# Kernel optimization log

Measured on AMD Instinct MI355X. Metric: run time of the kernel, lower is better.

Reference implementation:

```python
import jax, jax.numpy as jnp
import numpy as np

# dims
B, N, D = 4, 1024, 768
H, HD = 12, 64            # num_heads, head_dim (routed q heads = top-H experts)
EA = 24                   # num_attn_experts
EF, KF = 8, 2             # num_ffd_experts, ffd_heads (top-k for FFN MoE)
HS = int(4 * D) // KF     # ffn expert head_size = 1536
T = 9                     # task_num
S = 1                     # shared FFN experts: max(1, int(8*0.1))


def layernorm(x, g, b, eps=1e-5):
    m = x.mean(-1, keepdims=True)
    v = ((x - m) ** 2).mean(-1, keepdims=True)
    return (x - m) * jax.lax.rsqrt(v + eps) * g + b


def setup_inputs() -> dict:
    key = jax.random.key(0)
    ks = jax.random.split(key, 16)
    s = 0.02
    rn = lambda k, shp: jax.random.normal(k, shp, dtype=jnp.float32)
    return {
        "x": rn(ks[0], (B, N, D)),
        "task_bh": 3,
        "ln1_g": jnp.ones((D,), jnp.float32), "ln1_b": jnp.zeros((D,), jnp.float32),
        "ln2_g": jnp.ones((D,), jnp.float32), "ln2_b": jnp.zeros((D,), jnp.float32),
        "gate_a": rn(ks[1], (T, D, EA)) * s,
        "Wq_in": rn(ks[2], (EA, D, HD)) * s,
        "Wq_out": rn(ks[3], (EA, HD, D)) * s,
        "W_kv": rn(ks[4], (D, 2 * HD)) * s, "b_kv": jnp.zeros((2 * HD,), jnp.float32),
        "gate_f": rn(ks[5], (T, D, EF)) * s,
        "W1f": rn(ks[6], (EF, D, HS)) * s, "b1f": jnp.zeros((EF, HS), jnp.float32),
        "W2f": rn(ks[7], (EF, HS, D)) * s, "b_out": jnp.zeros((D,), jnp.float32),
        "Ws1": rn(ks[8], (S, D, HS)) * s, "bs1": jnp.zeros((S, HS), jnp.float32),
        "Ws2": rn(ks[9], (S, HS, D)) * s,
    }


def _route(h, gate_w, k):
    # h: [B,N,D], gate_w: [D,E] -> normalized top-k weights + one-hot dispatch
    probs = jax.nn.softmax(jnp.einsum("bnd,de->bne", h, gate_w), axis=-1)
    topv, topi = jax.lax.top_k(probs, k)                 # [B,N,k]
    topv = topv / topv.sum(-1, keepdims=True)
    oh = jax.nn.one_hot(topi, probs.shape[-1], dtype=h.dtype)  # [B,N,k,E]
    return topv, oh


def reference(x, task_bh, ln1_g, ln1_b, ln2_g, ln2_b, gate_a, Wq_in, Wq_out,
              W_kv, b_kv, gate_f, W1f, b1f, W2f, b_out, Ws1, bs1, Ws2):
    # --- MoE attention (routed q heads, shared single-head k/v) ---
    h = layernorm(x, ln1_g, ln1_b)
    topv, oh = _route(h, gate_a[task_bh], H)             # [B,N,H], [B,N,H,EA]
    h_all = jnp.einsum("bnd,edh->bneh", h, Wq_in)        # all-expert q projections
    q = jnp.einsum("bnke,bneh->bnkh", oh, h_all)         # gathered q heads [B,N,H,HD]
    kv = h @ W_kv + b_kv
    kk, vv = kv[..., :HD], kv[..., HD:]                  # [B,N,HD]
    att = jnp.einsum("bihd,bjd->bhij", q, kk) * (HD ** -0.5)
    att = jax.nn.softmax(att, axis=-1)
    o = jnp.einsum("bhij,bjd->bihd", att, vv)            # [B,N,H,HD]
    dense = jnp.einsum("bnk,bnke,bnkh->bneh", topv, oh, o)  # scatter to experts
    y = jnp.einsum("bneh,ehd->bnd", dense, Wq_out)       # gated expert output proj
    x = x + y

    # --- MoE FFN (top-KF routed experts + shared experts) ---
    h = layernorm(x, ln2_g, ln2_b)
    topv, oh = _route(h, gate_f[task_bh], KF)            # [B,N,KF], [B,N,KF,EF]
    h_all = jax.nn.gelu(jnp.einsum("bnd,edh->bneh", h, W1f) + b1f, approximate=False)
    wdense = jnp.einsum("bnk,bnke->bne", topv, oh)       # per-expert gate weights
    y = jnp.einsum("bne,bneh,ehd->bnd", wdense, h_all, W2f) + b_out
    hs = jax.nn.gelu(jnp.einsum("bnd,sdh->bnsh", h, Ws1) + bs1, approximate=False)
    y = y + jnp.einsum("bnsh,shd->bnd", hs, Ws2)         # always-on shared experts
    return x + y
```

## Files before the change

kernel.cpp:

```cpp
#include <hip/hip_runtime.h>
#include <hip/hip_bf16.h>

#define NTOK 4096
#define DDIM 768
#define NEA  24
#define NHEAD 12
#define HDIM 64
#define NEF  8
#define HSD  1536
#define SEQL 1024
#define NB   4
#define MAXTILE 104
#define NQKV 1664

using bf16 = __hip_bfloat16;

typedef float v4f __attribute__((ext_vector_type(4)));
typedef short v8s __attribute__((ext_vector_type(8)));
typedef __bf16 v8bf __attribute__((ext_vector_type(8)));

typedef __attribute__((address_space(3))) unsigned lds_u32_t;
typedef const __attribute__((address_space(1))) unsigned glb_u32_t;

__device__ __forceinline__ void gload16(const void* g, void* l) {
  __builtin_amdgcn_global_load_lds((glb_u32_t*)g, (lds_u32_t*)l, 16, 0, 0);
}

__device__ __forceinline__ float gelu_f(float x) {
  return 0.5f * x * (1.0f + erff(x * 0.70710678118654752440f));
}

__device__ __forceinline__ short f2bf_s(float x) {
  bf16 h = __float2bfloat16(x);
  return __builtin_bit_cast(short, h);
}

__device__ __forceinline__ int xcd_swz(int lin, int nwg) {
  return (lin & 7) * (nwg >> 3) + (lin >> 3);
}

__device__ __forceinline__ void gemm_core(const short* gA0, const short* gA1,
                                          const short* gB0, const short* gB1,
                                          short* lA, short* lB, int steps,
                                          v4f (&acc)[4][4])
{
  const int tid = threadIdx.x;
  const int w = tid >> 6, l = tid & 63;
  const int wr = (w >> 1) * 64, wc = (w & 1) * 64;
  const int fr = l & 15, ko = (l >> 4) * 8;
  const int sb = w * 1024;
  gload16(gA0, lA + sb); gload16(gA1, lA + sb + 512);
  gload16(gB0, lB + sb); gload16(gB1, lB + sb + 512);
  gA0 += 32; gA1 += 32; gB0 += 32; gB1 += 32;
  __syncthreads();
  int cur = 0;
  for (int s = 0; s < steps; ++s) {
    const int nxt = cur ^ 1;
    if (s + 1 < steps) {
      gload16(gA0, lA + nxt * 4096 + sb);
      gload16(gA1, lA + nxt * 4096 + sb + 512);
      gload16(gB0, lB + nxt * 4096 + sb);
      gload16(gB1, lB + nxt * 4096 + sb + 512);
      gA0 += 32; gA1 += 32; gB0 += 32; gB1 += 32;
    }
    const short* bA = lA + cur * 4096;
    const short* bB = lB + cur * 4096;
    v8s av[4], bv[4];
#pragma unroll
    for (int mi = 0; mi < 4; ++mi)
      av[mi] = *(const v8s*)(bA + (wr + mi * 16 + fr) * 32 + ko);
#pragma unroll
    for (int ni = 0; ni < 4; ++ni)
      bv[ni] = *(const v8s*)(bB + (wc + ni * 16 + fr) * 32 + ko);
#pragma unroll
    for (int mi = 0; mi < 4; ++mi)
#pragma unroll
      for (int ni = 0; ni < 4; ++ni)
        acc[mi][ni] = __builtin_amdgcn_mfma_f32_16x16x32_bf16(
            __builtin_bit_cast(v8bf, av[mi]), __builtin_bit_cast(v8bf, bv[ni]),
            acc[mi][ni], 0, 0, 0);
    __syncthreads();
    cur = nxt;
  }
}

template<int EPI>
__global__ __launch_bounds__(256, 4) void k_gemm(const short* __restrict__ A,
    const short* __restrict__ Bt, float* __restrict__ C,
    const float* __restrict__ addsrc, int N, int K)
{
  const int nwg = gridDim.x * gridDim.y;
  const int swz = xcd_swz(blockIdx.x + gridDim.x * blockIdx.y, nwg);
  const int m0 = (swz % gridDim.x) * 128, n0 = (swz / gridDim.x) * 128;
  __shared__ __align__(16) short lA[2 * 128 * 32];
  __shared__ __align__(16) short lB[2 * 128 * 32];
  const int tid = threadIdx.x, w = tid >> 6, l = tid & 63;
  const int ca = w * 128 + l, cb = ca + 64;
  const short* gA0 = A + (size_t)(m0 + (ca >> 2)) * K + (ca & 3) * 8;
  const short* gA1 = A + (size_t)(m0 + (cb >> 2)) * K + (cb & 3) * 8;
  const short* gB0 = Bt + (size_t)(n0 + (ca >> 2)) * K + (ca & 3) * 8;
  const short* gB1 = Bt + (size_t)(n0 + (cb >> 2)) * K + (cb & 3) * 8;
  v4f acc[4][4];
  v4f z = {0.f, 0.f, 0.f, 0.f};
#pragma unroll
  for (int i = 0; i < 4; ++i)
#pragma unroll
    for (int j = 0; j < 4; ++j) acc[i][j] = z;
  gemm_core(gA0, gA1, gB0, gB1, lA, lB, K >> 5, acc);
  const int wr = (w >> 1) * 64, wc = (w & 1) * 64;
  const int fr = l & 15, rq = (l >> 4) * 4;
#pragma unroll
  for (int mi = 0; mi < 4; ++mi)
#pragma unroll
    for (int ni = 0; ni < 4; ++ni)
#pragma unroll
      for (int j = 0; j < 4; ++j) {
        int rg = m0 + wr + mi * 16 + rq + j;
        int cg = n0 + wc + ni * 16 + fr;
        float v = acc[mi][ni][j];
        if (EPI == 2) v += addsrc[(size_t)rg * N + cg];
        C[(size_t)rg * N + cg] = v;
      }
}

template<int PHASE>
__global__ __launch_bounds__(256, 5) void k_gemm_moe(
    const short* __restrict__ Aact, const short* __restrict__ Wt,
    const short* __restrict__ Wst, const float* __restrict__ b1f,
    const float* __restrict__ bs1, const float* __restrict__ wsl,
    const int* __restrict__ off, const int* __restrict__ cnt,
    const int* __restrict__ list, const int* __restrict__ tmeta,
    const int* __restrict__ ntl, short* __restrict__ outb,
    float* __restrict__ outf)
{
  constexpr int K = (PHASE == 0) ? DDIM : HSD;
  constexpr int N = (PHASE == 0) ? HSD : DDIM;
  const int nwg = gridDim.x * gridDim.y;
  const int swz = xcd_swz(blockIdx.x + gridDim.x * blockIdx.y, nwg);
  const int ti = swz % gridDim.x;
  const int n0 = (swz / gridDim.x) * 128;
  if (ti >= ntl[0]) return;
  const int mm = tmeta[ti];
  const int e = mm >> 20;
  const int r0 = mm & 0xFFFFF;
  const int base = (e < 8) ? off[e] : NTOK * 2;
  const int c    = (e < 8) ? cnt[e] : NTOK;
  const int rows = c - r0;
  const short* Bt = (e < 8) ? Wt + (size_t)e * N * K : Wst;
  __shared__ __align__(16) short lA[2 * 128 * 32];
  __shared__ __align__(16) short lB[2 * 128 * 32];
  const int tid = threadIdx.x, w = tid >> 6, l = tid & 63;
  const int ca = w * 128 + l, cb = ca + 64;

  auto arowptr = [&](int chunk) -> const short* {
    int r = chunk >> 2;
    int re = (r < rows) ? r : (rows - 1);
    int slot = base + r0 + re;
    if (PHASE == 0) {
      int tok = (e < 8) ? list[slot] : (slot - NTOK * 2);
      return Aact + (size_t)tok * DDIM;
    } else {
      return Aact + (size_t)slot * HSD;
    }
  };
  const short* gA0 = arowptr(ca) + (ca & 3) * 8;
  const short* gA1 = arowptr(cb) + (cb & 3) * 8;
  const short* gB0 = Bt + (size_t)(n0 + (ca >> 2)) * K + (ca & 3) * 8;
  const short* gB1 = Bt + (size_t)(n0 + (cb >> 2)) * K + (cb & 3) * 8;
  v4f acc[4][4];
  v4f z = {0.f, 0.f, 0.f, 0.f};
#pragma unroll
  for (int i = 0; i < 4; ++i)
#pragma unroll
    for (int j = 0; j < 4; ++j) acc[i][j] = z;
  gemm_core(gA0, gA1, gB0, gB1, lA, lB, K >> 5, acc);
  const int wr = (w >> 1) * 64, wc = (w & 1) * 64;
  const int fr = l & 15, rq = (l >> 4) * 4;
  const float* bias = (PHASE == 0) ? ((e < 8) ? b1f + e * HSD : bs1) : nullptr;
#pragma unroll
  for (int mi = 0; mi < 4; ++mi)
#pragma unroll
    for (int ni = 0; ni < 4; ++ni)
#pragma unroll
      for (int j = 0; j < 4; ++j) {
        int rl = wr + mi * 16 + rq + j;
        if (rl >= rows) continue;
        int slot = base + r0 + rl;
        int cg = n0 + wc + ni * 16 + fr;
        float v = acc[mi][ni][j];
        if (PHASE == 0) {
          v = gelu_f(v + bias[cg]);
          outb[(size_t)slot * HSD + cg] = f2bf_s(v);
        } else {
          outf[(size_t)slot * DDIM + cg] = v * wsl[slot];
        }
      }
}

__global__ __launch_bounds__(256) void k_ln(const float* __restrict__ x,
    const float* __restrict__ g, const float* __restrict__ b,
    float* __restrict__ hf, bf16* __restrict__ hb)
{
  const size_t t = blockIdx.x;
  const float* xr = x + t * DDIM;
  int tid = threadIdx.x;
  float v0 = xr[tid], v1 = xr[tid + 256], v2 = xr[tid + 512];
  float s = v0 + v1 + v2;
  float q = v0 * v0 + v1 * v1 + v2 * v2;
  for (int m = 32; m >= 1; m >>= 1) { s += __shfl_xor(s, m); q += __shfl_xor(q, m); }
  __shared__ float rs[4], rq[4];
  int w = tid >> 6, l = tid & 63;
  if (l == 0) { rs[w] = s; rq[w] = q; }
  __syncthreads();
  s = rs[0] + rs[1] + rs[2] + rs[3];
  q = rq[0] + rq[1] + rq[2] + rq[3];
  float mean = s * (1.f / DDIM);
  float var = q * (1.f / DDIM) - mean * mean;
  float inv = rsqrtf(var + 1e-5f);
  float vv[3] = {v0, v1, v2};
#pragma unroll
  for (int i = 0; i < 3; ++i) {
    int d = tid + i * 256;
    float y = (vv[i] - mean) * inv * g[d] + b[d];
    hf[t * DDIM + d] = y;
    hb[t * DDIM + d] = __float2bfloat16(y);
  }
}

__global__ __launch_bounds__(256) void k_routeA(const float* __restrict__ hf,
    const float* __restrict__ gt, int* __restrict__ topi, float* __restrict__ topv)
{
  const int t = blockIdx.x * 4 + (threadIdx.x >> 6);
  const int l = threadIdx.x & 63;
  const float* h = hf + (size_t)t * DDIM;
  float hr[12];
#pragma unroll
  for (int m = 0; m < 12; ++m) hr[m] = h[l + 64 * m];
  float lg[NEA];
#pragma unroll
  for (int e = 0; e < NEA; ++e) {
    const float* ge = gt + e * DDIM;
    float a = 0.f;
#pragma unroll
    for (int m = 0; m < 12; ++m) a += hr[m] * ge[l + 64 * m];
#pragma unroll
    for (int m = 32; m >= 1; m >>= 1) a += __shfl_xor(a, m);
    lg[e] = a;
  }
  unsigned used = 0;
  int sel[NHEAD]; float bvk[NHEAD];
#pragma unroll
  for (int k = 0; k < NHEAD; ++k) {
    float bv = -3e30f; int best = 0;
#pragma unroll
    for (int e = 0; e < NEA; ++e)
      if (!((used >> e) & 1u) && lg[e] > bv) { bv = lg[e]; best = e; }
    used |= 1u << best; sel[k] = best; bvk[k] = bv;
  }
  const float mx = bvk[0];
  float pvk[NHEAD], ssum = 0.f;
#pragma unroll
  for (int k = 0; k < NHEAD; ++k) { pvk[k] = expf(bvk[k] - mx); ssum += pvk[k]; }
  const float inv = 1.f / ssum;
  if (l == 0) {
#pragma unroll
    for (int k = 0; k < NHEAD; ++k) {
      topi[t * NHEAD + k] = sel[k];
      topv[t * NHEAD + k] = pvk[k] * inv;
    }
  }
}

__global__ __launch_bounds__(256) void k_routeF(const float* __restrict__ hf,
    const float* __restrict__ gt, int* __restrict__ ef, float* __restrict__ wf,
    int* __restrict__ cnt)
{
  const int t = blockIdx.x * 4 + (threadIdx.x >> 6);
  const int l = threadIdx.x & 63;
  const float* h = hf + (size_t)t * DDIM;
  float hr[12];
#pragma unroll
  for (int m = 0; m < 12; ++m) hr[m] = h[l + 64 * m];
  float lg[NEF];
#pragma unroll
  for (int e = 0; e < NEF; ++e) {
    const float* ge = gt + e * DDIM;
    float a = 0.f;
#pragma unroll
    for (int m = 0; m < 12; ++m) a += hr[m] * ge[l + 64 * m];
#pragma unroll
    for (int m = 32; m >= 1; m >>= 1) a += __shfl_xor(a, m);
    lg[e] = a;
  }
  unsigned used = 0;
  int sel[2]; float bvk[2];
#pragma unroll
  for (int k = 0; k < 2; ++k) {
    float bv = -3e30f; int best = 0;
#pragma unroll
    for (int e = 0; e < NEF; ++e)
      if (!((used >> e) & 1u) && lg[e] > bv) { bv = lg[e]; best = e; }
    used |= 1u << best; sel[k] = best; bvk[k] = bv;
  }
  const float mx = bvk[0];
  float p0 = expf(bvk[0] - mx), p1 = expf(bvk[1] - mx);
  const float inv = 1.f / (p0 + p1);
  if (l == 0) {
    ef[t * 2 + 0] = sel[0]; wf[t * 2 + 0] = p0 * inv;
    ef[t * 2 + 1] = sel[1]; wf[t * 2 + 1] = p1 * inv;
    atomicAdd(&cnt[sel[0]], 1);
    atomicAdd(&cnt[sel[1]], 1);
  }
}

__global__ void k_packGT(const float* __restrict__ src, const int* __restrict__ task,
                         float* __restrict__ dst, int E)
{
  int idx = blockIdx.x * 256 + threadIdx.x;
  if (idx >= E * DDIM) return;
  int e = idx / DDIM, d = idx - e * DDIM;
  dst[idx] = src[(size_t)task[0] * DDIM * E + (size_t)d * E + e];
}

__global__ void k_off(const int* __restrict__ cnt, int* __restrict__ off,
                      int* __restrict__ cur, int* __restrict__ tmeta,
                      int* __restrict__ ntl)
{
  if (threadIdx.x == 0 && blockIdx.x == 0) {
    int a = 0;
    for (int e = 0; e < NEF; ++e) { off[e] = a; cur[e] = a; a += cnt[e]; }
    off[NEF] = a;
    int n = 0;
    for (int e = 0; e < NEF; ++e)
      for (int r = 0; r < cnt[e]; r += 128) tmeta[n++] = (e << 20) | r;
    for (int r = 0; r < NTOK; r += 128) tmeta[n++] = (8 << 20) | r;
    ntl[0] = n;
  }
}

__global__ void k_fill(const int* __restrict__ ef, const float* __restrict__ wf,
                       int* __restrict__ cur, int* __restrict__ list,
                       float* __restrict__ wsl, int* __restrict__ sof)
{
  int t = blockIdx.x * 256 + threadIdx.x;
  if (t >= NTOK) return;
  for (int k = 0; k < 2; ++k) {
    int e = ef[t * 2 + k];
    int slot = atomicAdd(&cur[e], 1);
    list[slot] = t;
    wsl[slot] = wf[t * 2 + k];
    sof[t * 2 + k] = slot;
  }
  list[NTOK * 2 + t] = t;
  wsl[NTOK * 2 + t] = 1.f;
}

__global__ void k_qgather(const float* __restrict__ hallq, const int* __restrict__ topi,
                          bf16* __restrict__ q)
{
  int idx = blockIdx.x * 256 + threadIdx.x;
  int t = idx / (NHEAD * HDIM);
  int rem = idx - t * (NHEAD * HDIM);
  int k = rem >> 6, hd = rem & 63;
  q[idx] = __float2bfloat16(
      hallq[(size_t)t * NQKV + topi[t * NHEAD + k] * HDIM + hd]);
}

__global__ void k_packKV(const float* __restrict__ hallq, const float* __restrict__ bkv,
                         bf16* __restrict__ kvb)
{
  int idx = blockIdx.x * 256 + threadIdx.x;
  int t = idx >> 7, j = idx & 127;
  kvb[idx] = __float2bfloat16(hallq[(size_t)t * NQKV + 1536 + j] + bkv[j]);
}

__global__ void k_scatter(const float* __restrict__ o, const int* __restrict__ topi,
                          const float* __restrict__ topv, bf16* __restrict__ dense)
{
  int idx = blockIdx.x * 256 + threadIdx.x;
  int t = idx / (NHEAD * HDIM);
  int rem = idx - t * (NHEAD * HDIM);
  int k = rem >> 6, hd = rem & 63;
  float v = topv[t * NHEAD + k] * o[idx];
  dense[(size_t)t * (NEA * HDIM) + topi[t * NHEAD + k] * HDIM + hd] = __float2bfloat16(v);
}

__global__ __launch_bounds__(256, 2) void k_attn_mfma(const bf16* __restrict__ q,
    const bf16* __restrict__ kv, float* __restrict__ o)
{
  __shared__ __align__(16) short Qs[64 * 64];
  __shared__ __align__(16) short Ks[64 * 64];
  __shared__ __align__(16) short Vs[64 * 64];
  __shared__ __align__(16) short Ps[64 * 64];
  const int i0 = blockIdx.x * 64;
  const int h = blockIdx.y;
  const int b = blockIdx.z;
  const int tid = threadIdx.x;
  const int w = tid >> 6, l = tid & 63;
  const int g = l >> 4, fq = l & 15;
  const short* qg = (const short*)q;
  const short* kvg = (const short*)kv;

  {
    int c0 = tid, c1 = tid + 256;
    int r0 = c0 >> 3, s0 = (c0 & 7) ^ (r0 & 7);
    int r1 = c1 >> 3, s1 = (c1 & 7) ^ (r1 & 7);
    gload16(qg + ((size_t)((b * SEQL + i0 + r0) * NHEAD + h)) * HDIM + s0 * 8,
            Qs + w * 512);
    gload16(qg + ((size_t)((b * SEQL + i0 + r1) * NHEAD + h)) * HDIM + s1 * 8,
            Qs + 2048 + w * 512);
  }

  float m_run[4], l_run[4];
  v4f oacc[4];
#pragma unroll
  for (int r = 0; r < 4; ++r) { m_run[r] = -1e30f; l_run[r] = 0.f; }
#pragma unroll
  for (int nd = 0; nd < 4; ++nd) oacc[nd] = (v4f){0.f, 0.f, 0.f, 0.f};

  const int vj = tid & 63;
  const int vd0 = (tid >> 6) * 16;

  for (int jt = 0; jt < 16; ++jt) {
    if (jt) __syncthreads();
    {
      int c0 = tid, c1 = tid + 256;
      int r0 = c0 >> 3, s0 = (c0 & 7) ^ (r0 & 7);
      int r1 = c1 >> 3, s1 = (c1 & 7) ^ (r1 & 7);
      gload16(kvg + ((size_t)(b * SEQL + jt * 64 + r0)) * 128 + s0 * 8,
              Ks + w * 512);
      gload16(kvg + ((size_t)(b * SEQL + jt * 64 + r1)) * 128 + s1 * 8,
              Ks + 2048 + w * 512);
    }
    {
      const short* gv = kvg + ((size_t)(b * SEQL + jt * 64 + vj)) * 128 + 64 + vd0;
      v8s a0 = *(const v8s*)gv;
      v8s a1 = *(const v8s*)(gv + 8);
#pragma unroll
      for (int k2 = 0; k2 < 8; ++k2) {
        int d = vd0 + k2;
        Vs[d * 64 + (((vj >> 3) ^ (d & 7)) << 3) + (vj & 7)] = a0[k2];
      }
#pragma unroll
      for (int k2 = 0; k2 < 8; ++k2) {
        int d = vd0 + 8 + k2;
        Vs[d * 64 + (((vj >> 3) ^ (d & 7)) << 3) + (vj & 7)] = a1[k2];
      }
    }
    __syncthreads();

    v8s aq[2];
#pragma unroll
    for (int kk = 0; kk < 2; ++kk)
      aq[kk] = *(const v8s*)&Qs[(16 * w + fq) * 64 + (((kk * 4 + g) ^ (fq & 7)) << 3)];
    v4f sacc[4];
#pragma unroll
    for (int n = 0; n < 4; ++n) {
      sacc[n] = (v4f){0.f, 0.f, 0.f, 0.f};
#pragma unroll
      for (int kk = 0; kk < 2; ++kk) {
        v8s bk = *(const v8s*)&Ks[(16 * n + fq) * 64 + (((kk * 4 + g) ^ (fq & 7)) << 3)];
        sacc[n] = __builtin_amdgcn_mfma_f32_16x16x32_bf16(
            __builtin_bit_cast(v8bf, aq[kk]), __builtin_bit_cast(v8bf, bk),
            sacc[n], 0, 0, 0);
      }
    }
#pragma unroll
    for (int n = 0; n < 4; ++n) sacc[n] *= 0.125f;

#pragma unroll
    for (int r = 0; r < 4; ++r) {
      float mt = fmaxf(fmaxf(sacc[0][r], sacc[1][r]), fmaxf(sacc[2][r], sacc[3][r]));
      mt = fmaxf(mt, __shfl_xor(mt, 1));
      mt = fmaxf(mt, __shfl_xor(mt, 2));
      mt = fmaxf(mt, __shfl_xor(mt, 4));
      mt = fmaxf(mt, __shfl_xor(mt, 8));
      float mnew = fmaxf(m_run[r], mt);
      float corr = __expf(m_run[r] - mnew);
      float pv[4], ps = 0.f;
#pragma unroll
      for (int n = 0; n < 4; ++n) { pv[n] = __expf(sacc[n][r] - mnew); ps += pv[n]; }
      ps += __shfl_xor(ps, 1);
      ps += __shfl_xor(ps, 2);
      ps += __shfl_xor(ps, 4);
      ps += __shfl_xor(ps, 8);
      l_run[r] = l_run[r] * corr + ps;
      m_run[r] = mnew;
#pragma unroll
      for (int nd = 0; nd < 4; ++nd) oacc[nd][r] *= corr;
      int qrow = 16 * w + 4 * g + r;
#pragma unroll
      for (int n = 0; n < 4; ++n)
        Ps[qrow * 64 + (((2 * n + (fq >> 3)) ^ (qrow & 7)) << 3) + (fq & 7)] =
            f2bf_s(pv[n]);
    }
    asm volatile("s_waitcnt lgkmcnt(0)" ::: "memory");
    __builtin_amdgcn_sched_barrier(0);

#pragma unroll
    for (int kk = 0; kk < 2; ++kk) {
      v8s pa = *(const v8s*)&Ps[(16 * w + fq) * 64 + (((kk * 4 + g) ^ (fq & 7)) << 3)];
#pragma unroll
      for (int nd = 0; nd < 4; ++nd) {
        v8s vb = *(const v8s*)&Vs[(16 * nd + fq) * 64 + (((kk * 4 + g) ^ (fq & 7)) << 3)];
        oacc[nd] = __builtin_amdgcn_mfma_f32_16x16x32_bf16(
            __builtin_bit_cast(v8bf, pa), __builtin_bit_cast(v8bf, vb),
            oacc[nd], 0, 0, 0);
      }
    }
  }

#pragma unroll
  for (int r = 0; r < 4; ++r) {
    float inv = 1.f / l_run[r];
    int qgl = i0 + 16 * w + 4 * g + r;
#pragma unroll
    for (int nd = 0; nd < 4; ++nd)
      o[(((size_t)b * SEQL + qgl) * NHEAD + h) * HDIM + 16 * nd + fq] =
          oacc[nd][r] * inv;
  }
}

__global__ __launch_bounds__(256) void k_packT(const float* __restrict__ src,
                                               bf16* __restrict__ dst, int K, int N)
{
  __shared__ float tile[32][33];
  const size_t zoff = (size_t)blockIdx.z * K * N;
  const int k0 = blockIdx.x * 32, n0 = blockIdx.y * 32;
  const int tx = threadIdx.x & 31, ty = threadIdx.x >> 5;
#pragma unroll
  for (int i = 0; i < 32; i += 8)
    tile[ty + i][tx] = src[zoff + (size_t)(k0 + ty + i) * N + n0 + tx];
  __syncthreads();
#pragma unroll
  for (int i = 0; i < 32; i += 8)
    dst[zoff + (size_t)(n0 + ty + i) * K + k0 + tx] =
        __float2bfloat16(tile[tx][ty + i]);
}

__global__ void k_final(const float* __restrict__ x2, const float* __restrict__ bout,
                        const float* __restrict__ yp, const int* __restrict__ sof,
                        float* __restrict__ out)
{
  int idx = blockIdx.x * 256 + threadIdx.x;
  int t = idx / DDIM, d = idx - t * DDIM;
  int s0 = sof[2 * t], s1 = sof[2 * t + 1];
  out[idx] = x2[idx] + bout[d] + yp[(size_t)s0 * DDIM + d] + yp[(size_t)s1 * DDIM + d] +
             yp[((size_t)(NTOK * 2) + t) * DDIM + d];
}

extern "C" void kernel_launch(void* const* d_in, const int* in_sizes, int n_in,
                              void* d_out, int out_size, void* d_ws, size_t ws_size,
                              hipStream_t stream) {
  const float* x      = (const float*)d_in[0];
  const int*   task   = (const int*)d_in[1];
  const float* ln1g   = (const float*)d_in[2];
  const float* ln1b   = (const float*)d_in[3];
  const float* ln2g   = (const float*)d_in[4];
  const float* ln2b   = (const float*)d_in[5];
  const float* gate_a = (const float*)d_in[6];
  const float* wq_in  = (const float*)d_in[7];
  const float* wq_out = (const float*)d_in[8];
  const float* w_kv   = (const float*)d_in[9];
  const float* b_kv   = (const float*)d_in[10];
  const float* gate_f = (const float*)d_in[11];
  const float* w1f    = (const float*)d_in[12];
  const float* b1f    = (const float*)d_in[13];
  const float* w2f    = (const float*)d_in[14];
  const float* b_out  = (const float*)d_in[15];
  const float* ws1    = (const float*)d_in[16];
  const float* bs1    = (const float*)d_in[17];
  const float* ws2    = (const float*)d_in[18];

  char* W = (char*)d_ws;
  size_t off_ = 0;
  auto alloc = [&](size_t b) { size_t o = off_; off_ += (b + 255) & ~(size_t)255; return o; };
  size_t o_h1f   = alloc(12582912);
  size_t o_h1b   = alloc(6291456);
  size_t o_hallq = alloc(27262976);
  size_t o_hmid  = o_h1f;
  size_t o_q     = alloc(12582912);
  size_t o_o     = alloc(12582912);
  size_t o_dense = alloc(12582912);
  size_t o_ypart = o_q;
  size_t o_kvb   = alloc(1048576);
  size_t o_x2    = alloc(12582912);
  size_t o_h2f   = alloc(12582912);
  size_t o_h2b   = alloc(6291456);
  size_t o_btq   = alloc(2555904);
  size_t o_wqot  = alloc(2359296);
  size_t o_w1t   = alloc(18874368);
  size_t o_w2t   = alloc(18874368);
  size_t o_ws1t  = alloc(2359296);
  size_t o_ws2t  = alloc(2359296);
  size_t o_topi  = alloc(196608);
  size_t o_topv  = alloc(196608);
  size_t o_ef    = alloc(32768);
  size_t o_wf    = alloc(32768);
  size_t o_cnt   = alloc(1024);
  size_t o_offs  = alloc(1024);
  size_t o_cur   = alloc(1024);
  size_t o_list  = alloc(49152);
  size_t o_wsl   = alloc(49152);
  size_t o_sof   = alloc(32768);
  size_t o_tmeta = alloc(1024);
  size_t o_ntl   = alloc(256);
  size_t o_gta   = alloc(73728);
  size_t o_gtf   = alloc(24576);
  if (ws_size < off_) return;

  float* h1f   = (float*)(W + o_h1f);
  bf16*  h1b   = (bf16*)(W + o_h1b);
  float* hallq = (float*)(W + o_hallq);
  bf16*  qbb   = (bf16*)(W + o_q);
  float* ob    = (float*)(W + o_o);
  bf16*  dense = (bf16*)(W + o_dense);
  bf16*  kvbb  = (bf16*)(W + o_kvb);
  float* x2b   = (float*)(W + o_x2);
  float* h2f   = (float*)(W + o_h2f);
  bf16*  h2b   = (bf16*)(W + o_h2b);
  short* hmid  = (short*)(W + o_hmid);
  float* ypart = (float*)(W + o_ypart);
  int*   topi  = (int*)(W + o_topi);
  float* topv  = (float*)(W + o_topv);
  int*   efp   = (int*)(W + o_ef);
  float* wfp   = (float*)(W + o_wf);
  int*   cntp  = (int*)(W + o_cnt);
  int*   offp  = (int*)(W + o_offs);
  int*   curp  = (int*)(W + o_cur);
  int*   listp = (int*)(W + o_list);
  float* wslp  = (float*)(W + o_wsl);
  int*   sofp  = (int*)(W + o_sof);
  int*   tmeta = (int*)(W + o_tmeta);
  int*   ntl   = (int*)(W + o_ntl);
  float* gta   = (float*)(W + o_gta);
  float* gtf   = (float*)(W + o_gtf);

  k_packT<<<dim3(24, 2, 24), 256, 0, stream>>>(wq_in, (bf16*)(W + o_btq), 768, 64);
  k_packT<<<dim3(24, 4, 1), 256, 0, stream>>>(w_kv, (bf16*)(W + o_btq) + 1536 * 768, 768, 128);
  k_packT<<<dim3(48, 24, 1), 256, 0, stream>>>(wq_out, (bf16*)(W + o_wqot), 1536, 768);
  k_packT<<<dim3(24, 48, 8), 256, 0, stream>>>(w1f, (bf16*)(W + o_w1t), 768, 1536);
  k_packT<<<dim3(48, 24, 8), 256, 0, stream>>>(w2f, (bf16*)(W + o_w2t), 1536, 768);
  k_packT<<<dim3(24, 48, 1), 256, 0, stream>>>(ws1, (bf16*)(W + o_ws1t), 768, 1536);
  k_packT<<<dim3(48, 24, 1), 256, 0, stream>>>(ws2, (bf16*)(W + o_ws2t), 1536, 768);
  k_packGT<<<dim3(72), 256, 0, stream>>>(gate_a, task, gta, NEA);
  k_packGT<<<dim3(24), 256, 0, stream>>>(gate_f, task, gtf, NEF);

  (void)hipMemsetAsync(W + o_dense, 0, 12582912, stream);
  (void)hipMemsetAsync(W + o_cnt, 0, 64, stream);

  k_ln<<<NTOK, 256, 0, stream>>>(x, ln1g, ln1b, h1f, h1b);
  k_routeA<<<NTOK / 4, 256, 0, stream>>>(h1f, gta, topi, topv);

  k_gemm<0><<<dim3(32, 13), 256, 0, stream>>>((const short*)h1b, (const short*)(W + o_btq),
                                              hallq, nullptr, NQKV, 768);

  k_qgather<<<dim3(12288), 256, 0, stream>>>(hallq, topi, qbb);
  k_packKV<<<dim3(2048), 256, 0, stream>>>(hallq, b_kv, kvbb);
  k_attn_mfma<<<dim3(16, NHEAD, NB), 256, 0, stream>>>(qbb, kvbb, ob);
  k_scatter<<<dim3(12288), 256, 0, stream>>>(ob, topi, topv, dense);

  k_gemm<2><<<dim3(32, 6), 256, 0, stream>>>((const short*)dense, (const short*)(W + o_wqot),
                                             x2b, x, 768, 1536);

  k_ln<<<NTOK, 256, 0, stream>>>(x2b, ln2g, ln2b, h2f, h2b);
  k_routeF<<<NTOK / 4, 256, 0, stream>>>(h2f, gtf, efp, wfp, cntp);
  k_off<<<1, 1, 0, stream>>>(cntp, offp, curp, tmeta, ntl);
  k_fill<<<16, 256, 0, stream>>>(efp, wfp, curp, listp, wslp, sofp);

  k_gemm_moe<0><<<dim3(MAXTILE, 12), 256, 0, stream>>>((const short*)h2b,
      (const short*)(W + o_w1t), (const short*)(W + o_ws1t), b1f, bs1, nullptr,
      offp, cntp, listp, tmeta, ntl, hmid, nullptr);
  k_gemm_moe<1><<<dim3(MAXTILE, 6), 256, 0, stream>>>((const short*)hmid,
      (const short*)(W + o_w2t), (const short*)(W + o_ws2t), nullptr, nullptr, wslp,
      offp, cntp, listp, tmeta, ntl, nullptr, ypart);

  k_final<<<dim3(12288), 256, 0, stream>>>(x2b, b_out, ypart, sofp, (float*)d_out);
}
```

Before: 558.7 us.

## Double GEMM K-tile to 64 with XOR-swizzled LDS layout

Replaces the shared GEMM core with one that stages 64-wide K slices per step instead of 32, halving the number of barrier-separated iterations. The global-to-LDS source addresses are XOR-swizzled by row so the MFMA fragment reads avoid LDS bank conflicts. LDS use doubles to 64 KB per block, and launch bounds drop to 2 waves per SIMD, which lowers occupancy in exchange for fewer syncs and more MFMA work per stage.

```diff
diff --git a/kernel.cpp b/kernel.cpp
--- a/kernel.cpp
+++ b/kernel.cpp
@@ -39,74 +39,90 @@
   return (lin & 7) * (nwg >> 3) + (lin >> 3);
 }
 
-__device__ __forceinline__ void gemm_core(const short* gA0, const short* gA1,
-                                          const short* gB0, const short* gB1,
-                                          short* lA, short* lB, int steps,
-                                          v4f (&acc)[4][4])
+__device__ __forceinline__ void gemm_core64(
+    const short* gA0, const short* gA1, const short* gA2, const short* gA3,
+    const short* gB0, const short* gB1, const short* gB2, const short* gB3,
+    short* lA, short* lB, int steps, v4f (&acc)[4][4])
 {
   const int tid = threadIdx.x;
   const int w = tid >> 6, l = tid & 63;
   const int wr = (w >> 1) * 64, wc = (w & 1) * 64;
-  const int fr = l & 15, ko = (l >> 4) * 8;
-  const int sb = w * 1024;
-  gload16(gA0, lA + sb); gload16(gA1, lA + sb + 512);
-  gload16(gB0, lB + sb); gload16(gB1, lB + sb + 512);
-  gA0 += 32; gA1 += 32; gB0 += 32; gB1 += 32;
+  const int fr = l & 15, g = l >> 4;
+  auto stage = [&](int buf) {
+    short* bA = lA + buf * 8192 + w * 512;
+    short* bB = lB + buf * 8192 + w * 512;
+    gload16(gA0, bA);        gload16(gA1, bA + 2048);
+    gload16(gA2, bA + 4096); gload16(gA3, bA + 6144);
+    gload16(gB0, bB);        gload16(gB1, bB + 2048);
+    gload16(gB2, bB + 4096); gload16(gB3, bB + 6144);
+    gA0 += 64; gA1 += 64; gA2 += 64; gA3 += 64;
+    gB0 += 64; gB1 += 64; gB2 += 64; gB3 += 64;
+  };
+  stage(0);
   __syncthreads();
   int cur = 0;
   for (int s = 0; s < steps; ++s) {
     const int nxt = cur ^ 1;
-    if (s + 1 < steps) {
-      gload16(gA0, lA + nxt * 4096 + sb);
-      gload16(gA1, lA + nxt * 4096 + sb + 512);
-      gload16(gB0, lB + nxt * 4096 + sb);
-      gload16(gB1, lB + nxt * 4096 + sb + 512);
-      gA0 += 32; gA1 += 32; gB0 += 32; gB1 += 32;
-    }
-    const short* bA = lA + cur * 4096;
-    const short* bB = lB + cur * 4096;
-    v8s av[4], bv[4];
-#pragma unroll
-    for (int mi = 0; mi < 4; ++mi)
-      av[mi] = *(const v8s*)(bA + (wr + mi * 16 + fr) * 32 + ko);
-#pragma unroll
-    for (int ni = 0; ni < 4; ++ni)
-      bv[ni] = *(const v8s*)(bB + (wc + ni * 16 + fr) * 32 + ko);
-#pragma unroll
-    for (int mi = 0; mi < 4; ++mi)
-#pragma unroll
-      for (int ni = 0; ni < 4; ++ni)
-        acc[mi][ni] = __builtin_amdgcn_mfma_f32_16x16x32_bf16(
-            __builtin_bit_cast(v8bf, av[mi]), __builtin_bit_cast(v8bf, bv[ni]),
-            acc[mi][ni], 0, 0, 0);
+    if (s + 1 < steps) stage(nxt);
+    const short* bA = lA + cur * 8192;
+    const short* bB = lB + cur * 8192;
+    v8s av[4][2], bv[4][2];
+#pragma unroll
+    for (int mi = 0; mi < 4; ++mi) {
+      int r = wr + mi * 16 + fr;
+#pragma unroll
+      for (int kk = 0; kk < 2; ++kk)
+        av[mi][kk] = *(const v8s*)(bA + r * 64 + (((kk * 4 + g) ^ (fr & 7)) << 3));
+    }
+#pragma unroll
+    for (int ni = 0; ni < 4; ++ni) {
+      int r = wc + ni * 16 + fr;
+#pragma unroll
+      for (int kk = 0; kk < 2; ++kk)
+        bv[ni][kk] = *(const v8s*)(bB + r * 64 + (((kk * 4 + g) ^ (fr & 7)) << 3));
+    }
+#pragma unroll
+    for (int kk = 0; kk < 2; ++kk)
+#pragma unroll
+      for (int mi = 0; mi < 4; ++mi)
+#pragma unroll
+        for (int ni = 0; ni < 4; ++ni)
+          acc[mi][ni] = __builtin_amdgcn_mfma_f32_16x16x32_bf16(
+              __builtin_bit_cast(v8bf, av[mi][kk]), __builtin_bit_cast(v8bf, bv[ni][kk]),
+              acc[mi][ni], 0, 0, 0);
     __syncthreads();
     cur = nxt;
   }
 }
 
 template<int EPI>
-__global__ __launch_bounds__(256, 4) void k_gemm(const short* __restrict__ A,
+__global__ __launch_bounds__(256, 2) void k_gemm(const short* __restrict__ A,
     const short* __restrict__ Bt, float* __restrict__ C,
     const float* __restrict__ addsrc, int N, int K)
 {
   const int nwg = gridDim.x * gridDim.y;
   const int swz = xcd_swz(blockIdx.x + gridDim.x * blockIdx.y, nwg);
   const int m0 = (swz % gridDim.x) * 128, n0 = (swz / gridDim.x) * 128;
-  __shared__ __align__(16) short lA[2 * 128 * 32];
-  __shared__ __align__(16) short lB[2 * 128 * 32];
+  __shared__ __align__(16) short lA[2 * 128 * 64];
+  __shared__ __align__(16) short lB[2 * 128 * 64];
   const int tid = threadIdx.x, w = tid >> 6, l = tid & 63;
-  const int ca = w * 128 + l, cb = ca + 64;
-  const short* gA0 = A + (size_t)(m0 + (ca >> 2)) * K + (ca & 3) * 8;
-  const short* gA1 = A + (size_t)(m0 + (cb >> 2)) * K + (cb & 3) * 8;
-  const short* gB0 = Bt + (size_t)(n0 + (ca >> 2)) * K + (ca & 3) * 8;
-  const short* gB1 = Bt + (size_t)(n0 + (cb >> 2)) * K + (cb & 3) * 8;
+  const short* gA[4];
+  const short* gB[4];
+#pragma unroll
+  for (int i = 0; i < 4; ++i) {
+    int c = tid + 256 * i;
+    int r = c >> 3, s8 = (c & 7) ^ (r & 7);
+    gA[i] = A + (size_t)(m0 + r) * K + s8 * 8;
+    gB[i] = Bt + (size_t)(n0 + r) * K + s8 * 8;
+  }
   v4f acc[4][4];
   v4f z = {0.f, 0.f, 0.f, 0.f};
 #pragma unroll
   for (int i = 0; i < 4; ++i)
 #pragma unroll
     for (int j = 0; j < 4; ++j) acc[i][j] = z;
-  gemm_core(gA0, gA1, gB0, gB1, lA, lB, K >> 5, acc);
+  gemm_core64(gA[0], gA[1], gA[2], gA[3], gB[0], gB[1], gB[2], gB[3],
+              lA, lB, K >> 6, acc);
   const int wr = (w >> 1) * 64, wc = (w & 1) * 64;
   const int fr = l & 15, rq = (l >> 4) * 4;
 #pragma unroll
@@ -124,7 +140,7 @@
 }
 
 template<int PHASE>
-__global__ __launch_bounds__(256, 5) void k_gemm_moe(
+__global__ __launch_bounds__(256, 2) void k_gemm_moe(
     const short* __restrict__ Aact, const short* __restrict__ Wt,
     const short* __restrict__ Wst, const float* __restrict__ b1f,
     const float* __restrict__ bs1, const float* __restrict__ wsl,
@@ -147,13 +163,11 @@
   const int c    = (e < 8) ? cnt[e] : NTOK;
   const int rows = c - r0;
   const short* Bt = (e < 8) ? Wt + (size_t)e * N * K : Wst;
-  __shared__ __align__(16) short lA[2 * 128 * 32];
-  __shared__ __align__(16) short lB[2 * 128 * 32];
+  __shared__ __align__(16) short lA[2 * 128 * 64];
+  __shared__ __align__(16) short lB[2 * 128 * 64];
   const int tid = threadIdx.x, w = tid >> 6, l = tid & 63;
-  const int ca = w * 128 + l, cb = ca + 64;
-
-  auto arowptr = [&](int chunk) -> const short* {
-    int r = chunk >> 2;
+
+  auto arowptr = [&](int r) -> const short* {
     int re = (r < rows) ? r : (rows - 1);
     int slot = base + r0 + re;
     if (PHASE == 0) {
@@ -163,17 +177,23 @@
       return Aact + (size_t)slot * HSD;
     }
   };
-  const short* gA0 = arowptr(ca) + (ca & 3) * 8;
-  const short* gA1 = arowptr(cb) + (cb & 3) * 8;
-  const short* gB0 = Bt + (size_t)(n0 + (ca >> 2)) * K + (ca & 3) * 8;
-  const short* gB1 = Bt + (size_t)(n0 + (cb >> 2)) * K + (cb & 3) * 8;
+  const short* gA[4];
+  const short* gB[4];
+#pragma unroll
+  for (int i = 0; i < 4; ++i) {
+    int cch = tid + 256 * i;
+    int r = cch >> 3, s8 = (cch & 7) ^ (r & 7);
+    gA[i] = arowptr(r) + s8 * 8;
+    gB[i] = Bt + (size_t)(n0 + r) * K + s8 * 8;
+  }
   v4f acc[4][4];
   v4f z = {0.f, 0.f, 0.f, 0.f};
 #pragma unroll
   for (int i = 0; i < 4; ++i)
 #pragma unroll
     for (int j = 0; j < 4; ++j) acc[i][j] = z;
-  gemm_core(gA0, gA1, gB0, gB1, lA, lB, K >> 5, acc);
+  gemm_core64(gA[0], gA[1], gA[2], gA[3], gB[0], gB[1], gB[2], gB[3],
+              lA, lB, K >> 6, acc);
   const int wr = (w >> 1) * 64, wc = (w & 1) * 64;
   const int fr = l & 15, rq = (l >> 4) * 4;
   const float* bias = (PHASE == 0) ? ((e < 8) ? b1f + e * HSD : bs1) : nullptr;
```

New measurement: 588.3 us. 1.05x slower.

## Replace MoE FFN GEMM with single-wave 64x64 tile kernel

Applied to the files above, without the earlier changes.

Swaps the 256-thread 128x128-tile MoE FFN GEMM for a 64-thread kernel where one wavefront computes a 64x64 tile, with its own double-buffered global-to-LDS load loop. Row tiles per expert drop from 128 to 64, which cuts padding waste on ragged expert segments and yields many more workgroups for load balance. In exchange, each tile reuses data less, so more global and LDS traffic is spent per FLOP, and a single wave per workgroup has fewer warps to hide latency.

```diff
diff --git a/kernel.cpp b/kernel.cpp
--- a/kernel.cpp
+++ b/kernel.cpp
@@ -10,7 +10,7 @@
 #define HSD  1536
 #define SEQL 1024
 #define NB   4
-#define MAXTILE 104
+#define MAXT64 200
 #define NQKV 1664
 
 using bf16 = __hip_bfloat16;
@@ -124,7 +124,7 @@
 }
 
 template<int PHASE>
-__global__ __launch_bounds__(256, 5) void k_gemm_moe(
+__global__ __launch_bounds__(64) void k_moe1w(
     const short* __restrict__ Aact, const short* __restrict__ Wt,
     const short* __restrict__ Wst, const float* __restrict__ b1f,
     const float* __restrict__ bs1, const float* __restrict__ wsl,
@@ -138,7 +138,7 @@
   const int nwg = gridDim.x * gridDim.y;
   const int swz = xcd_swz(blockIdx.x + gridDim.x * blockIdx.y, nwg);
   const int ti = swz % gridDim.x;
-  const int n0 = (swz / gridDim.x) * 128;
+  const int n0 = (swz / gridDim.x) * 64;
   if (ti >= ntl[0]) return;
   const int mm = tmeta[ti];
   const int e = mm >> 20;
@@ -147,35 +147,77 @@
   const int c    = (e < 8) ? cnt[e] : NTOK;
   const int rows = c - r0;
   const short* Bt = (e < 8) ? Wt + (size_t)e * N * K : Wst;
-  __shared__ __align__(16) short lA[2 * 128 * 32];
-  __shared__ __align__(16) short lB[2 * 128 * 32];
-  const int tid = threadIdx.x, w = tid >> 6, l = tid & 63;
-  const int ca = w * 128 + l, cb = ca + 64;
-
-  auto arowptr = [&](int chunk) -> const short* {
-    int r = chunk >> 2;
+  __shared__ __align__(16) short lA[2 * 64 * 32];
+  __shared__ __align__(16) short lB[2 * 64 * 32];
+  const int l = threadIdx.x;
+
+  auto arowptr = [&](int r) -> const short* {
     int re = (r < rows) ? r : (rows - 1);
     int slot = base + r0 + re;
     if (PHASE == 0) {
       int tok = (e < 8) ? list[slot] : (slot - NTOK * 2);
       return Aact + (size_t)tok * DDIM;
-    } else {
-      return Aact + (size_t)slot * HSD;
-    }
+    }
+    return Aact + (size_t)slot * HSD;
   };
-  const short* gA0 = arowptr(ca) + (ca & 3) * 8;
-  const short* gA1 = arowptr(cb) + (cb & 3) * 8;
-  const short* gB0 = Bt + (size_t)(n0 + (ca >> 2)) * K + (ca & 3) * 8;
-  const short* gB1 = Bt + (size_t)(n0 + (cb >> 2)) * K + (cb & 3) * 8;
+  const short* gA[4];
+  const short* gB[4];
+#pragma unroll
+  for (int i = 0; i < 4; ++i) {
+    int ch = i * 64 + l;
+    int r = ch >> 2, c8 = (ch & 3) * 8;
+    gA[i] = arowptr(r) + c8;
+    gB[i] = Bt + (size_t)(n0 + r) * K + c8;
+  }
   v4f acc[4][4];
   v4f z = {0.f, 0.f, 0.f, 0.f};
 #pragma unroll
   for (int i = 0; i < 4; ++i)
 #pragma unroll
     for (int j = 0; j < 4; ++j) acc[i][j] = z;
-  gemm_core(gA0, gA1, gB0, gB1, lA, lB, K >> 5, acc);
-  const int wr = (w >> 1) * 64, wc = (w & 1) * 64;
-  const int fr = l & 15, rq = (l >> 4) * 4;
+
+  asm volatile("s_waitcnt vmcnt(0)" ::: "memory");
+
+  auto stage = [&](int buf) {
+    short* bA = lA + buf * 2048;
+    short* bB = lB + buf * 2048;
+#pragma unroll
+    for (int i = 0; i < 4; ++i) { gload16(gA[i], bA + i * 512); gA[i] += 32; }
+#pragma unroll
+    for (int i = 0; i < 4; ++i) { gload16(gB[i], bB + i * 512); gB[i] += 32; }
+  };
+  const int steps = K >> 5;
+  const int fr = l & 15, ko = (l >> 4) * 8;
+  stage(0);
+  int cur = 0;
+  for (int s = 0; s < steps; ++s) {
+    if (s + 1 < steps) {
+      stage(cur ^ 1);
+      asm volatile("s_waitcnt vmcnt(8)" ::: "memory");
+    } else {
+      asm volatile("s_waitcnt vmcnt(0)" ::: "memory");
+    }
+    __builtin_amdgcn_sched_barrier(0);
+    const short* bA = lA + cur * 2048;
+    const short* bB = lB + cur * 2048;
+    v8s av[4], bv[4];
+#pragma unroll
+    for (int mi = 0; mi < 4; ++mi)
+      av[mi] = *(const v8s*)(bA + (mi * 16 + fr) * 32 + ko);
+#pragma unroll
+    for (int ni = 0; ni < 4; ++ni)
+      bv[ni] = *(const v8s*)(bB + (ni * 16 + fr) * 32 + ko);
+#pragma unroll
+    for (int mi = 0; mi < 4; ++mi)
+#pragma unroll
+      for (int ni = 0; ni < 4; ++ni)
+        acc[mi][ni] = __builtin_amdgcn_mfma_f32_16x16x32_bf16(
+            __builtin_bit_cast(v8bf, av[mi]), __builtin_bit_cast(v8bf, bv[ni]),
+            acc[mi][ni], 0, 0, 0);
+    cur ^= 1;
+  }
+
+  const int rq = (l >> 4) * 4;
   const float* bias = (PHASE == 0) ? ((e < 8) ? b1f + e * HSD : bs1) : nullptr;
 #pragma unroll
   for (int mi = 0; mi < 4; ++mi)
@@ -183,10 +225,10 @@
     for (int ni = 0; ni < 4; ++ni)
 #pragma unroll
       for (int j = 0; j < 4; ++j) {
-        int rl = wr + mi * 16 + rq + j;
+        int rl = mi * 16 + rq + j;
         if (rl >= rows) continue;
         int slot = base + r0 + rl;
-        int cg = n0 + wc + ni * 16 + fr;
+        int cg = n0 + ni * 16 + fr;
         float v = acc[mi][ni][j];
         if (PHASE == 0) {
           v = gelu_f(v + bias[cg]);
@@ -332,8 +374,8 @@
     off[NEF] = a;
     int n = 0;
     for (int e = 0; e < NEF; ++e)
-      for (int r = 0; r < cnt[e]; r += 128) tmeta[n++] = (e << 20) | r;
-    for (int r = 0; r < NTOK; r += 128) tmeta[n++] = (8 << 20) | r;
+      for (int r = 0; r < cnt[e]; r += 64) tmeta[n++] = (e << 20) | r;
+    for (int r = 0; r < NTOK; r += 64) tmeta[n++] = (8 << 20) | r;
     ntl[0] = n;
   }
 }
@@ -668,10 +710,10 @@
   k_off<<<1, 1, 0, stream>>>(cntp, offp, curp, tmeta, ntl);
   k_fill<<<16, 256, 0, stream>>>(efp, wfp, curp, listp, wslp, sofp);
 
-  k_gemm_moe<0><<<dim3(MAXTILE, 12), 256, 0, stream>>>((const short*)h2b,
+  k_moe1w<0><<<dim3(MAXT64, 24), 64, 0, stream>>>((const short*)h2b,
       (const short*)(W + o_w1t), (const short*)(W + o_ws1t), b1f, bs1, nullptr,
       offp, cntp, listp, tmeta, ntl, hmid, nullptr);
-  k_gemm_moe<1><<<dim3(MAXTILE, 6), 256, 0, stream>>>((const short*)hmid,
+  k_moe1w<1><<<dim3(MAXT64, 12), 64, 0, stream>>>((const short*)hmid,
       (const short*)(W + o_w2t), (const short*)(W + o_ws2t), nullptr, nullptr, wslp,
       offp, cntp, listp, tmeta, ntl, nullptr, ypart);
 
```

New measurement: 627.0 us. 1.12x slower.

## Fuse layernorm into routing kernels and gather Q directly inside attention

Applied to the files above, without the earlier changes.

Merges each layernorm with its routing kernel so one wavefront per token computes the statistics, writes the bf16 normalized row and computes the gate logits, with no fp32 intermediate. The QKV GEMM now writes bf16 output, and the attention kernel gathers the routed q heads through topi, which removes the separate q-gather kernel and its buffer. Workspace regions are reorganized to match. The bf16 rounding of the k/v projection before the bias is added introduces a little extra precision loss.

```diff
diff --git a/kernel.cpp b/kernel.cpp
--- a/kernel.cpp
+++ b/kernel.cpp
@@ -86,7 +86,7 @@
 
 template<int EPI>
 __global__ __launch_bounds__(256, 4) void k_gemm(const short* __restrict__ A,
-    const short* __restrict__ Bt, float* __restrict__ C,
+    const short* __restrict__ Bt, float* __restrict__ C, bf16* __restrict__ Cb,
     const float* __restrict__ addsrc, int N, int K)
 {
   const int nwg = gridDim.x * gridDim.y;
@@ -119,7 +119,8 @@
         int cg = n0 + wc + ni * 16 + fr;
         float v = acc[mi][ni][j];
         if (EPI == 2) v += addsrc[(size_t)rg * N + cg];
-        C[(size_t)rg * N + cg] = v;
+        if (EPI == 3) Cb[(size_t)rg * N + cg] = __float2bfloat16(v);
+        else          C[(size_t)rg * N + cg] = v;
       }
 }
 
@@ -197,45 +198,32 @@
       }
 }
 
-__global__ __launch_bounds__(256) void k_ln(const float* __restrict__ x,
-    const float* __restrict__ g, const float* __restrict__ b,
-    float* __restrict__ hf, bf16* __restrict__ hb)
-{
-  const size_t t = blockIdx.x;
-  const float* xr = x + t * DDIM;
-  int tid = threadIdx.x;
-  float v0 = xr[tid], v1 = xr[tid + 256], v2 = xr[tid + 512];
-  float s = v0 + v1 + v2;
-  float q = v0 * v0 + v1 * v1 + v2 * v2;
-  for (int m = 32; m >= 1; m >>= 1) { s += __shfl_xor(s, m); q += __shfl_xor(q, m); }
-  __shared__ float rs[4], rq[4];
-  int w = tid >> 6, l = tid & 63;
-  if (l == 0) { rs[w] = s; rq[w] = q; }
-  __syncthreads();
-  s = rs[0] + rs[1] + rs[2] + rs[3];
-  q = rq[0] + rq[1] + rq[2] + rq[3];
-  float mean = s * (1.f / DDIM);
-  float var = q * (1.f / DDIM) - mean * mean;
-  float inv = rsqrtf(var + 1e-5f);
-  float vv[3] = {v0, v1, v2};
-#pragma unroll
-  for (int i = 0; i < 3; ++i) {
-    int d = tid + i * 256;
-    float y = (vv[i] - mean) * inv * g[d] + b[d];
-    hf[t * DDIM + d] = y;
-    hb[t * DDIM + d] = __float2bfloat16(y);
-  }
-}
-
-__global__ __launch_bounds__(256) void k_routeA(const float* __restrict__ hf,
-    const float* __restrict__ gt, int* __restrict__ topi, float* __restrict__ topv)
+__global__ __launch_bounds__(256) void k_lnrouteA(const float* __restrict__ x,
+    const float* __restrict__ lg_, const float* __restrict__ lb_,
+    const float* __restrict__ gt, bf16* __restrict__ hb,
+    int* __restrict__ topi, float* __restrict__ topv)
 {
   const int t = blockIdx.x * 4 + (threadIdx.x >> 6);
   const int l = threadIdx.x & 63;
-  const float* h = hf + (size_t)t * DDIM;
+  const float* xr = x + (size_t)t * DDIM;
+  float v[12];
+  float s = 0.f, q = 0.f;
+#pragma unroll
+  for (int m = 0; m < 12; ++m) {
+    v[m] = xr[l + 64 * m];
+    s += v[m]; q += v[m] * v[m];
+  }
+#pragma unroll
+  for (int m = 32; m >= 1; m >>= 1) { s += __shfl_xor(s, m); q += __shfl_xor(q, m); }
+  const float mean = s * (1.f / DDIM);
+  const float inv = rsqrtf(q * (1.f / DDIM) - mean * mean + 1e-5f);
   float hr[12];
 #pragma unroll
-  for (int m = 0; m < 12; ++m) hr[m] = h[l + 64 * m];
+  for (int m = 0; m < 12; ++m) {
+    int d = l + 64 * m;
+    hr[m] = (v[m] - mean) * inv * lg_[d] + lb_[d];
+    hb[(size_t)t * DDIM + d] = __float2bfloat16(hr[m]);
+  }
   float lg[NEA];
 #pragma unroll
   for (int e = 0; e < NEA; ++e) {
@@ -261,26 +249,42 @@
   float pvk[NHEAD], ssum = 0.f;
 #pragma unroll
   for (int k = 0; k < NHEAD; ++k) { pvk[k] = expf(bvk[k] - mx); ssum += pvk[k]; }
-  const float inv = 1.f / ssum;
+  const float invs = 1.f / ssum;
   if (l == 0) {
 #pragma unroll
     for (int k = 0; k < NHEAD; ++k) {
       topi[t * NHEAD + k] = sel[k];
-      topv[t * NHEAD + k] = pvk[k] * inv;
-    }
-  }
-}
-
-__global__ __launch_bounds__(256) void k_routeF(const float* __restrict__ hf,
-    const float* __restrict__ gt, int* __restrict__ ef, float* __restrict__ wf,
-    int* __restrict__ cnt)
+      topv[t * NHEAD + k] = pvk[k] * invs;
+    }
+  }
+}
+
+__global__ __launch_bounds__(256) void k_lnrouteF(const float* __restrict__ x,
+    const float* __restrict__ lg_, const float* __restrict__ lb_,
+    const float* __restrict__ gt, bf16* __restrict__ hb,
+    int* __restrict__ ef, float* __restrict__ wf, int* __restrict__ cnt)
 {
   const int t = blockIdx.x * 4 + (threadIdx.x >> 6);
   const int l = threadIdx.x & 63;
-  const float* h = hf + (size_t)t * DDIM;
+  const float* xr = x + (size_t)t * DDIM;
+  float v[12];
+  float s = 0.f, q = 0.f;
+#pragma unroll
+  for (int m = 0; m < 12; ++m) {
+    v[m] = xr[l + 64 * m];
+    s += v[m]; q += v[m] * v[m];
+  }
+#pragma unroll
+  for (int m = 32; m >= 1; m >>= 1) { s += __shfl_xor(s, m); q += __shfl_xor(q, m); }
+  const float mean = s * (1.f / DDIM);
+  const float inv = rsqrtf(q * (1.f / DDIM) - mean * mean + 1e-5f);
   float hr[12];
 #pragma unroll
-  for (int m = 0; m < 12; ++m) hr[m] = h[l + 64 * m];
+  for (int m = 0; m < 12; ++m) {
+    int d = l + 64 * m;
+    hr[m] = (v[m] - mean) * inv * lg_[d] + lb_[d];
+    hb[(size_t)t * DDIM + d] = __float2bfloat16(hr[m]);
+  }
   float lg[NEF];
 #pragma unroll
   for (int e = 0; e < NEF; ++e) {
@@ -304,10 +308,10 @@
   }
   const float mx = bvk[0];
   float p0 = expf(bvk[0] - mx), p1 = expf(bvk[1] - mx);
-  const float inv = 1.f / (p0 + p1);
+  const float invs = 1.f / (p0 + p1);
   if (l == 0) {
-    ef[t * 2 + 0] = sel[0]; wf[t * 2 + 0] = p0 * inv;
-    ef[t * 2 + 1] = sel[1]; wf[t * 2 + 1] = p1 * inv;
+    ef[t * 2 + 0] = sel[0]; wf[t * 2 + 0] = p0 * invs;
+    ef[t * 2 + 1] = sel[1]; wf[t * 2 + 1] = p1 * invs;
     atomicAdd(&cnt[sel[0]], 1);
     atomicAdd(&cnt[sel[1]], 1);
   }
@@ -355,23 +359,13 @@
   wsl[NTOK * 2 + t] = 1.f;
 }
 
-__global__ void k_qgather(const float* __restrict__ hallq, const int* __restrict__ topi,
-                          bf16* __restrict__ q)
-{
-  int idx = blockIdx.x * 256 + threadIdx.x;
-  int t = idx / (NHEAD * HDIM);
-  int rem = idx - t * (NHEAD * HDIM);
-  int k = rem >> 6, hd = rem & 63;
-  q[idx] = __float2bfloat16(
-      hallq[(size_t)t * NQKV + topi[t * NHEAD + k] * HDIM + hd]);
-}
-
-__global__ void k_packKV(const float* __restrict__ hallq, const float* __restrict__ bkv,
+__global__ void k_packKV(const bf16* __restrict__ hq, const float* __restrict__ bkv,
                          bf16* __restrict__ kvb)
 {
   int idx = blockIdx.x * 256 + threadIdx.x;
   int t = idx >> 7, j = idx & 127;
-  kvb[idx] = __float2bfloat16(hallq[(size_t)t * NQKV + 1536 + j] + bkv[j]);
+  float v = __bfloat162float(hq[(size_t)t * NQKV + 1536 + j]) + bkv[j];
+  kvb[idx] = __float2bfloat16(v);
 }
 
 __global__ void k_scatter(const float* __restrict__ o, const int* __restrict__ topi,
@@ -385,8 +379,8 @@
   dense[(size_t)t * (NEA * HDIM) + topi[t * NHEAD + k] * HDIM + hd] = __float2bfloat16(v);
 }
 
-__global__ __launch_bounds__(256, 2) void k_attn_mfma(const bf16* __restrict__ q,
-    const bf16* __restrict__ kv, float* __restrict__ o)
+__global__ __launch_bounds__(256, 2) void k_attn_mfma(const bf16* __restrict__ hq,
+    const int* __restrict__ topi, const bf16* __restrict__ kv, float* __restrict__ o)
 {
   __shared__ __align__(16) short Qs[64 * 64];
   __shared__ __align__(16) short Ks[64 * 64];
@@ -398,17 +392,17 @@
   const int tid = threadIdx.x;
   const int w = tid >> 6, l = tid & 63;
   const int g = l >> 4, fq = l & 15;
-  const short* qg = (const short*)q;
+  const short* qg = (const short*)hq;
   const short* kvg = (const short*)kv;
 
   {
     int c0 = tid, c1 = tid + 256;
     int r0 = c0 >> 3, s0 = (c0 & 7) ^ (r0 & 7);
     int r1 = c1 >> 3, s1 = (c1 & 7) ^ (r1 & 7);
-    gload16(qg + ((size_t)((b * SEQL + i0 + r0) * NHEAD + h)) * HDIM + s0 * 8,
-            Qs + w * 512);
-    gload16(qg + ((size_t)((b * SEQL + i0 + r1) * NHEAD + h)) * HDIM + s1 * 8,
-            Qs + 2048 + w * 512);
+    int t0 = b * SEQL + i0 + r0, t1 = b * SEQL + i0 + r1;
+    int e0 = topi[t0 * NHEAD + h], e1 = topi[t1 * NHEAD + h];
+    gload16(qg + (size_t)t0 * NQKV + e0 * HDIM + s0 * 8, Qs + w * 512);
+    gload16(qg + (size_t)t1 * NQKV + e1 * HDIM + s1 * 8, Qs + 2048 + w * 512);
   }
 
   float m_run[4], l_run[4];
@@ -575,17 +569,16 @@
   char* W = (char*)d_ws;
   size_t off_ = 0;
   auto alloc = [&](size_t b) { size_t o = off_; off_ += (b + 255) & ~(size_t)255; return o; };
-  size_t o_h1f   = alloc(12582912);
-  size_t o_h1b   = alloc(6291456);
-  size_t o_hallq = alloc(27262976);
-  size_t o_hmid  = o_h1f;
+  size_t o_reg1  = alloc(37748736);
+  size_t o_h1b   = o_reg1;
+  size_t o_hallq = o_reg1 + 6291456;
+  size_t o_hmid  = o_reg1;
   size_t o_q     = alloc(12582912);
   size_t o_o     = alloc(12582912);
   size_t o_dense = alloc(12582912);
   size_t o_ypart = o_q;
   size_t o_kvb   = alloc(1048576);
   size_t o_x2    = alloc(12582912);
-  size_t o_h2f   = alloc(12582912);
   size_t o_h2b   = alloc(6291456);
   size_t o_btq   = alloc(2555904);
   size_t o_wqot  = alloc(2359296);
@@ -609,15 +602,12 @@
   size_t o_gtf   = alloc(24576);
   if (ws_size < off_) return;
 
-  float* h1f   = (float*)(W + o_h1f);
   bf16*  h1b   = (bf16*)(W + o_h1b);
-  float* hallq = (float*)(W + o_hallq);
-  bf16*  qbb   = (bf16*)(W + o_q);
+  bf16*  hallqb= (bf16*)(W + o_hallq);
   float* ob    = (float*)(W + o_o);
   bf16*  dense = (bf16*)(W + o_dense);
   bf16*  kvbb  = (bf16*)(W + o_kvb);
   float* x2b   = (float*)(W + o_x2);
-  float* h2f   = (float*)(W + o_h2f);
   bf16*  h2b   = (bf16*)(W + o_h2b);
   short* hmid  = (short*)(W + o_hmid);
   float* ypart = (float*)(W + o_ypart);
@@ -649,22 +639,19 @@
   (void)hipMemsetAsync(W + o_dense, 0, 12582912, stream);
   (void)hipMemsetAsync(W + o_cnt, 0, 64, stream);
 
-  k_ln<<<NTOK, 256, 0, stream>>>(x, ln1g, ln1b, h1f, h1b);
-  k_routeA<<<NTOK / 4, 256, 0, stream>>>(h1f, gta, topi, topv);
-
-  k_gemm<0><<<dim3(32, 13), 256, 0, stream>>>((const short*)h1b, (const short*)(W + o_btq),
-                                              hallq, nullptr, NQKV, 768);
-
-  k_qgather<<<dim3(12288), 256, 0, stream>>>(hallq, topi, qbb);
-  k_packKV<<<dim3(2048), 256, 0, stream>>>(hallq, b_kv, kvbb);
-  k_attn_mfma<<<dim3(16, NHEAD, NB), 256, 0, stream>>>(qbb, kvbb, ob);
+  k_lnrouteA<<<NTOK / 4, 256, 0, stream>>>(x, ln1g, ln1b, gta, h1b, topi, topv);
+
+  k_gemm<3><<<dim3(32, 13), 256, 0, stream>>>((const short*)h1b, (const short*)(W + o_btq),
+                                              nullptr, hallqb, nullptr, NQKV, 768);
+
+  k_packKV<<<dim3(2048), 256, 0, stream>>>(hallqb, b_kv, kvbb);
+  k_attn_mfma<<<dim3(16, NHEAD, NB), 256, 0, stream>>>(hallqb, topi, kvbb, ob);
   k_scatter<<<dim3(12288), 256, 0, stream>>>(ob, topi, topv, dense);
 
   k_gemm<2><<<dim3(32, 6), 256, 0, stream>>>((const short*)dense, (const short*)(W + o_wqot),
-                                             x2b, x, 768, 1536);
-
-  k_ln<<<NTOK, 256, 0, stream>>>(x2b, ln2g, ln2b, h2f, h2b);
-  k_routeF<<<NTOK / 4, 256, 0, stream>>>(h2f, gtf, efp, wfp, cntp);
+                                             x2b, nullptr, x, 768, 1536);
+
+  k_lnrouteF<<<NTOK / 4, 256, 0, stream>>>(x2b, ln2g, ln2b, gtf, h2b, efp, wfp, cntp);
   k_off<<<1, 1, 0, stream>>>(cntp, offp, curp, tmeta, ntl);
   k_fill<<<16, 256, 0, stream>>>(efp, wfp, curp, listp, wslp, sofp);
 
```

Result: faster. 532.4 us (-4.7%).
